# Performance work log

Measured on AMD Instinct MI355X. Metric: run time of the kernel, lower is better.

The kernel has to match this reference:

```python
import jax, jax.numpy as jnp
import numpy as np

B, CIN, COUT, WDIM, H, W = 16, 512, 3, 512, 128, 128
FC_GAIN = float(1.0 / np.sqrt(WDIM))        # FullyConnectedLayer weight gain (lr_mult=1)
WEIGHT_GAIN = float(1.0 / np.sqrt(CIN * 1))  # 1 / sqrt(in_channels * kernel_size**2)
CLAMP = 256.0


def setup_inputs() -> dict:
    key = jax.random.key(0)
    k = jax.random.split(key, 5)
    return {
        "x": jax.random.normal(k[0], (B, CIN, H, W), jnp.float32),
        "w": jax.random.normal(k[1], (B, WDIM), jnp.float32),
        # StyleSplit: FullyConnectedLayer(w_dim, 3*in_channels, bias_init=1)
        "affine_W": jax.random.normal(k[2], (3 * CIN, WDIM), jnp.float32),
        "affine_b": jnp.ones((3 * CIN,), jnp.float32),
        # 1x1 conv weight, init 0.1*randn, stored as [COUT, CIN]
        "conv_w": 0.1 * jax.random.normal(k[3], (COUT, CIN), jnp.float32),
        "conv_b": jnp.zeros((COUT,), jnp.float32),
    }


def reference(x, w, affine_W, affine_b, conv_w, conv_b):
    # StyleSplit affine: FC (with 1/sqrt(in) weight gain) -> m1*m2 + m3
    s = w @ affine_W.T * FC_GAIN + affine_b            # [B, 3*CIN]
    m1, m2, m3 = jnp.split(s, 3, axis=1)               # each [B, CIN]
    styles = (m1 * m2 + m3) * WEIGHT_GAIN              # [B, CIN]
    # Modulated 1x1 conv, demodulate=False: per-sample weight = conv_w * styles
    out = jnp.einsum('bchw,oc,bc->bohw', x, conv_w, styles)  # [B, COUT, H, W]
    # bias_act: linear activation + bias + clamp
    out = out + conv_b[None, :, None, None]
    return jnp.clip(out, -CLAMP, CLAMP)
```

## Files before the change

### kernel.cpp

```cpp
#include <hip/hip_runtime.h>
#include <hip/hip_bf16.h>

#define B_      16
#define CIN_    512
#define COUT_   3
#define WDIM_   512
#define HW_     16384
#define FC_GAIN     0.044194173824159216f
#define WEIGHT_GAIN 0.044194173824159216f
#define CLAMP_  256.0f

__global__ __launch_bounds__(64) void style_kernel(
    const float* __restrict__ w,
    const float* __restrict__ affine_W,
    const float* __restrict__ affine_b,
    const float* __restrict__ conv_w,
    float4* __restrict__ eff4) {
  const int bc   = blockIdx.x;
  const int b    = bc >> 9;
  const int c    = bc & 511;
  const int lane = threadIdx.x;

  const float* wb = w + b * WDIM_;
  const float* r1 = affine_W + (size_t)c * WDIM_;
  const float* r2 = affine_W + (size_t)(c + CIN_) * WDIM_;
  const float* r3 = affine_W + (size_t)(c + 2 * CIN_) * WDIM_;

  float p1 = 0.f, p2 = 0.f, p3 = 0.f;
#pragma unroll
  for (int j = 0; j < WDIM_ / 64; ++j) {
    const int k = j * 64 + lane;
    const float wk = wb[k];
    p1 = fmaf(wk, r1[k], p1);
    p2 = fmaf(wk, r2[k], p2);
    p3 = fmaf(wk, r3[k], p3);
  }
#pragma unroll
  for (int off = 32; off > 0; off >>= 1) {
    p1 += __shfl_down(p1, off);
    p2 += __shfl_down(p2, off);
    p3 += __shfl_down(p3, off);
  }
  if (lane == 0) {
    const float s1 = p1 * FC_GAIN + affine_b[c];
    const float s2 = p2 * FC_GAIN + affine_b[c + CIN_];
    const float s3 = p3 * FC_GAIN + affine_b[c + 2 * CIN_];
    const float style = (s1 * s2 + s3) * WEIGHT_GAIN;
    float4 e;
    e.x = conv_w[0 * CIN_ + c] * style;
    e.y = conv_w[1 * CIN_ + c] * style;
    e.z = conv_w[2 * CIN_ + c] * style;
    e.w = 0.f;
    eff4[bc] = e;
  }
}

__global__ __launch_bounds__(256) void conv_kernel(
    const float* __restrict__ x,
    const float4* __restrict__ eff4,
    const float* __restrict__ conv_b,
    float* __restrict__ out) {
  __shared__ float4 s_eff[CIN_];

  const int b    = blockIdx.x >> 4;
  const int tile = blockIdx.x & 15;
  const int tid  = threadIdx.x;

  s_eff[tid]       = eff4[b * CIN_ + tid];
  s_eff[tid + 256] = eff4[b * CIN_ + tid + 256];
  __syncthreads();

  const float4* xb = (const float4*)x + ((size_t)b * CIN_) * (HW_ / 4)
                     + (size_t)tile * 256 + tid;

  float a0x = 0.f, a0y = 0.f, a0z = 0.f, a0w = 0.f;
  float a1x = 0.f, a1y = 0.f, a1z = 0.f, a1w = 0.f;
  float a2x = 0.f, a2y = 0.f, a2z = 0.f, a2w = 0.f;

#pragma unroll 8
  for (int c = 0; c < CIN_; ++c) {
    const float4 xv = xb[(size_t)c * (HW_ / 4)];
    const float4 e  = s_eff[c];
    a0x = fmaf(xv.x, e.x, a0x); a0y = fmaf(xv.y, e.x, a0y);
    a0z = fmaf(xv.z, e.x, a0z); a0w = fmaf(xv.w, e.x, a0w);
    a1x = fmaf(xv.x, e.y, a1x); a1y = fmaf(xv.y, e.y, a1y);
    a1z = fmaf(xv.z, e.y, a1z); a1w = fmaf(xv.w, e.y, a1w);
    a2x = fmaf(xv.x, e.z, a2x); a2y = fmaf(xv.y, e.z, a2y);
    a2z = fmaf(xv.z, e.z, a2z); a2w = fmaf(xv.w, e.z, a2w);
  }

  const float b0 = conv_b[0], b1 = conv_b[1], b2 = conv_b[2];
#define CLMP(v, bb) fminf(fmaxf((v) + (bb), -CLAMP_), CLAMP_)
  float4 o0 = make_float4(CLMP(a0x, b0), CLMP(a0y, b0), CLMP(a0z, b0), CLMP(a0w, b0));
  float4 o1 = make_float4(CLMP(a1x, b1), CLMP(a1y, b1), CLMP(a1z, b1), CLMP(a1w, b1));
  float4 o2 = make_float4(CLMP(a2x, b2), CLMP(a2y, b2), CLMP(a2z, b2), CLMP(a2w, b2));
#undef CLMP

  float4* op = (float4*)out + ((size_t)b * COUT_) * (HW_ / 4)
               + (size_t)tile * 256 + tid;
  op[0]                = o0;
  op[1 * (HW_ / 4)]    = o1;
  op[2 * (HW_ / 4)]    = o2;
}

extern "C" void kernel_launch(void* const* d_in, const int* in_sizes, int n_in,
                              void* d_out, int out_size, void* d_ws, size_t ws_size,
                              hipStream_t stream) {
  const float* x        = (const float*)d_in[0];
  const float* w        = (const float*)d_in[1];
  const float* affine_W = (const float*)d_in[2];
  const float* affine_b = (const float*)d_in[3];
  const float* conv_w   = (const float*)d_in[4];
  const float* conv_b   = (const float*)d_in[5];
  float* out = (float*)d_out;

  float4* eff4 = (float4*)d_ws;

  style_kernel<<<B_ * CIN_, 64, 0, stream>>>(w, affine_W, affine_b, conv_w, eff4);
  conv_kernel<<<B_ * 16, 256, 0, stream>>>(x, eff4, conv_b, out);
}
```

Baseline: 672.7 us.

## Split channel reduction across four thread groups with shared-memory combine

The conv kernel now uses 1024-thread blocks, where four groups each reduce over 128 of the 512 input channels for the same pixel tile. Partial sums are combined through shared memory before bias and clamp are applied. This is meant to raise the number of in-flight memory loads, since the earlier grid of 256 blocks of 256 threads underfilled the GPU for this bandwidth-bound stream over x. The cost is extra shared memory, a second barrier and a reduction step.

```diff
diff --git a/kernel.cpp b/kernel.cpp
--- a/kernel.cpp
+++ b/kernel.cpp
@@ -6,6 +6,7 @@
 #define COUT_   3
 #define WDIM_   512
 #define HW_     16384
+#define HW4_    4096
 #define FC_GAIN     0.044194173824159216f
 #define WEIGHT_GAIN 0.044194173824159216f
 #define CLAMP_  256.0f
@@ -55,32 +56,36 @@
   }
 }
 
-__global__ __launch_bounds__(256) void conv_kernel(
+__global__ __launch_bounds__(1024) void conv_kernel(
     const float* __restrict__ x,
     const float4* __restrict__ eff4,
     const float* __restrict__ conv_b,
     float* __restrict__ out) {
   __shared__ float4 s_eff[CIN_];
+  __shared__ float4 s_red[3][4][256];
 
   const int b    = blockIdx.x >> 4;
   const int tile = blockIdx.x & 15;
   const int tid  = threadIdx.x;
+  const int grp  = tid >> 8;
+  const int px   = tid & 255;
 
-  s_eff[tid]       = eff4[b * CIN_ + tid];
-  s_eff[tid + 256] = eff4[b * CIN_ + tid + 256];
+  if (tid < CIN_) s_eff[tid] = eff4[b * CIN_ + tid];
   __syncthreads();
 
-  const float4* xb = (const float4*)x + ((size_t)b * CIN_) * (HW_ / 4)
-                     + (size_t)tile * 256 + tid;
+  const float4* xb = (const float4*)x
+      + ((size_t)(b * CIN_ + grp * 128)) * HW4_
+      + (size_t)tile * 256 + px;
+  const float4* ep = &s_eff[grp * 128];
 
   float a0x = 0.f, a0y = 0.f, a0z = 0.f, a0w = 0.f;
   float a1x = 0.f, a1y = 0.f, a1z = 0.f, a1w = 0.f;
   float a2x = 0.f, a2y = 0.f, a2z = 0.f, a2w = 0.f;
 
-#pragma unroll 8
-  for (int c = 0; c < CIN_; ++c) {
-    const float4 xv = xb[(size_t)c * (HW_ / 4)];
-    const float4 e  = s_eff[c];
+#pragma unroll 4
+  for (int c = 0; c < 128; ++c) {
+    const float4 xv = xb[(size_t)c * HW4_];
+    const float4 e  = ep[c];
     a0x = fmaf(xv.x, e.x, a0x); a0y = fmaf(xv.y, e.x, a0y);
     a0z = fmaf(xv.z, e.x, a0z); a0w = fmaf(xv.w, e.x, a0w);
     a1x = fmaf(xv.x, e.y, a1x); a1y = fmaf(xv.y, e.y, a1y);
@@ -89,18 +94,28 @@
     a2z = fmaf(xv.z, e.z, a2z); a2w = fmaf(xv.w, e.z, a2w);
   }
 
-  const float b0 = conv_b[0], b1 = conv_b[1], b2 = conv_b[2];
-#define CLMP(v, bb) fminf(fmaxf((v) + (bb), -CLAMP_), CLAMP_)
-  float4 o0 = make_float4(CLMP(a0x, b0), CLMP(a0y, b0), CLMP(a0z, b0), CLMP(a0w, b0));
-  float4 o1 = make_float4(CLMP(a1x, b1), CLMP(a1y, b1), CLMP(a1z, b1), CLMP(a1w, b1));
-  float4 o2 = make_float4(CLMP(a2x, b2), CLMP(a2y, b2), CLMP(a2z, b2), CLMP(a2w, b2));
+  s_red[0][grp][px] = make_float4(a0x, a0y, a0z, a0w);
+  s_red[1][grp][px] = make_float4(a1x, a1y, a1z, a1w);
+  s_red[2][grp][px] = make_float4(a2x, a2y, a2z, a2w);
+  __syncthreads();
+
+  if (tid < 768) {
+    const int o = tid >> 8;
+    const float4 v0 = s_red[o][0][px];
+    const float4 v1 = s_red[o][1][px];
+    const float4 v2 = s_red[o][2][px];
+    const float4 v3 = s_red[o][3][px];
+    const float bb = conv_b[o];
+#define CLMP(v) fminf(fmaxf((v) + bb, -CLAMP_), CLAMP_)
+    float4 ov = make_float4(CLMP(v0.x + v1.x + v2.x + v3.x),
+                            CLMP(v0.y + v1.y + v2.y + v3.y),
+                            CLMP(v0.z + v1.z + v2.z + v3.z),
+                            CLMP(v0.w + v1.w + v2.w + v3.w));
 #undef CLMP
-
-  float4* op = (float4*)out + ((size_t)b * COUT_) * (HW_ / 4)
-               + (size_t)tile * 256 + tid;
-  op[0]                = o0;
-  op[1 * (HW_ / 4)]    = o1;
-  op[2 * (HW_ / 4)]    = o2;
+    float4* op = (float4*)out + ((size_t)(b * COUT_ + o)) * HW4_
+                 + (size_t)tile * 256 + px;
+    *op = ov;
+  }
 }
 
 extern "C" void kernel_launch(void* const* d_in, const int* in_sizes, int n_in,
@@ -117,5 +132,5 @@
   float4* eff4 = (float4*)d_ws;
 
   style_kernel<<<B_ * CIN_, 64, 0, stream>>>(w, affine_W, affine_b, conv_w, eff4);
-  conv_kernel<<<B_ * 16, 256, 0, stream>>>(x, eff4, conv_b, out);
+  conv_kernel<<<B_ * 16, 1024, 0, stream>>>(x, eff4, conv_b, out);
 }
```

Result: no change. 673.6 us (+0.1%).
